# Kernel tuning notes

Hardware: AMD Instinct MI355X
Metric: run time of the kernel (lower is better)

The kernel has to match this reference:

```python
import jax, jax.numpy as jnp
import numpy as np

EXTENT = 1.0  # kernel-point influence radius (init kwarg 'extent')
B, N, M, H, K, F, C = 4, 16384, 16384, 32, 15, 64, 64


def setup_inputs() -> dict:
    key = jax.random.key(0)
    ks = jax.random.split(key, 6)
    points = jax.random.uniform(ks[0], (B, N, 3), dtype=jnp.float32)
    features = jax.random.normal(ks[1], (B, N, F), dtype=jnp.float32)
    output_points = jax.random.uniform(ks[2], (B, M, 3), dtype=jnp.float32)
    neighbor_indices = jax.random.randint(ks[3], (B, M, H), 0, N)
    # kernel point dispositions inside a ball of radius 1.5*extent (load_kernels stand-in)
    k_points = jax.random.uniform(ks[4], (K, 3), minval=-1.0, maxval=1.0, dtype=jnp.float32) * (1.5 * EXTENT) / jnp.sqrt(3.0)
    k_values = jax.random.normal(ks[5], (K, F, C), dtype=jnp.float32) * 0.05
    return {
        'points': points, 'features': features, 'output_points': output_points,
        'k_points': k_points, 'k_values': k_values, 'neighbor_indices': neighbor_indices,
    }


def reference(points, features, output_points, k_points, k_values, neighbor_indices):
    b, m, h = neighbor_indices.shape
    idx = neighbor_indices.reshape(b, m * h, 1)
    # batched gather (tf.gather batch_dims=1)
    neigh_pts = jnp.take_along_axis(points, idx, axis=1).reshape(b, m, h, 3)
    neigh_feat = jnp.take_along_axis(features, idx, axis=1).reshape(b, m, h, -1)
    # relative coords to each output point, then to each kernel point
    rel = neigh_pts - output_points[:, :, None, :]                # [B,M,H,3]
    diff = rel[:, :, :, None, :] - k_points                       # [B,M,H,K,3]
    sq_d = jnp.sum(diff * diff, axis=-1)                          # [B,M,H,K]
    # linear influence
    w = jnp.maximum(1.0 - jnp.sqrt(sq_d) / EXTENT, 0.0)           # [B,M,H,K]
    # weight neighbor features per kernel point, then apply per-kernel linear map, sum over K
    wf = jnp.einsum('bmhk,bmhf->bmkf', w, neigh_feat)             # [B,M,K,F]
    out = jnp.einsum('bmkf,kfc->bmc', wf, k_values)               # [B,M,C]
    return out
```

## Files before the change

### kernel.cpp

```cpp
#include <hip/hip_runtime.h>

#define BATCH 4
#define NPTS 16384
#define MPTS 16384
#define NH 32
#define NK 15
#define NF 64
#define NC 64
#define MT 16

typedef short short8 __attribute__((ext_vector_type(8)));
typedef float floatx4 __attribute__((ext_vector_type(4)));

__device__ __forceinline__ unsigned short f2bf(float x) {
    unsigned int u = __builtin_bit_cast(unsigned int, x);
    u = u + 0x7FFFu + ((u >> 16) & 1u);
    return (unsigned short)(u >> 16);
}

__device__ __forceinline__ unsigned pack_trunc(float lo, float hi) {
    return __builtin_amdgcn_perm(__builtin_bit_cast(unsigned, hi),
                                 __builtin_bit_cast(unsigned, lo), 0x07060302u);
}

__global__ void prep_kernel(const float* __restrict__ kv, const float* __restrict__ feat,
                            unsigned short* __restrict__ vp, unsigned short* __restrict__ featbf) {
    if (blockIdx.x < 32) {
        const int gid = blockIdx.x * 256 + threadIdx.x;
        const int lane = gid & 63;
        const int ct   = (gid >> 6) & 3;
        const int kk   = gid >> 8;
        const int c    = ct * 16 + (lane & 15);
        const int kap0 = kk * 32 + (lane >> 4) * 8;
        unsigned int o[4];
        #pragma unroll
        for (int jj = 0; jj < 4; jj++) {
            unsigned short lo, hi;
            {
                const int kap = kap0 + jj * 2;
                const int f = kap >> 4, k = kap & 15;
                lo = (k < NK) ? f2bf(kv[((size_t)(k * NF + f)) * NC + c]) : (unsigned short)0;
            }
            {
                const int kap = kap0 + jj * 2 + 1;
                const int f = kap >> 4, k = kap & 15;
                hi = (k < NK) ? f2bf(kv[((size_t)(k * NF + f)) * NC + c]) : (unsigned short)0;
            }
            o[jj] = (unsigned)lo | ((unsigned)hi << 16);
        }
        *(uint4*)(vp + (size_t)gid * 8) = make_uint4(o[0], o[1], o[2], o[3]);
    } else {
        const int gid = (blockIdx.x - 32) * 256 + threadIdx.x;
        const size_t base = (size_t)gid * 8;
        float4 a = *(const float4*)(feat + base);
        float4 b = *(const float4*)(feat + base + 4);
        uint4 o;
        o.x = (unsigned)f2bf(a.x) | ((unsigned)f2bf(a.y) << 16);
        o.y = (unsigned)f2bf(a.z) | ((unsigned)f2bf(a.w) << 16);
        o.z = (unsigned)f2bf(b.x) | ((unsigned)f2bf(b.y) << 16);
        o.w = (unsigned)f2bf(b.z) | ((unsigned)f2bf(b.w) << 16);
        *(uint4*)(featbf + base) = o;
    }
}

__global__ __launch_bounds__(256, 5) void kpconv_kernel(
    const float* __restrict__ points,
    const unsigned short* __restrict__ featbf,
    const float* __restrict__ outpts,
    const float* __restrict__ kpts,
    const unsigned short* __restrict__ vp,
    const int*   __restrict__ nbr,
    float* __restrict__ out)
{
    __shared__ __align__(16) unsigned short awf[16 * 512];
    __shared__ unsigned short feat_s[4 * 1288];
    __shared__ int   idx_s[512];
    __shared__ float opt_s[48];
    __shared__ float kp_s[48];

    const int tid   = threadIdx.x;
    const int batch = blockIdx.x >> 10;
    const int m0    = (blockIdx.x & 1023) << 4;

    if (tid < 48) kp_s[tid] = (tid < 45) ? kpts[tid] : 1e9f;
    if (tid >= 64 && tid < 112)
        opt_s[tid - 64] = outpts[(size_t)(batch * MPTS + m0) * 3 + (tid - 64)];
    {
        const size_t nb = (size_t)(batch * MPTS + m0) * NH;
        idx_s[tid]       = nbr[nb + tid];
        idx_s[256 + tid] = nbr[nb + 256 + tid];
    }
    __syncthreads();

    const int g    = tid >> 6;
    const int lane = tid & 63;
    const int cl   = lane & 15;
    const int q    = lane >> 4;
    const int sa   = cl;
    const int sfc  = q;

    const unsigned short* fbase = featbf + (size_t)(batch * NPTS) * NF;

    uint4 pra, prb;
    {
        const int srow = g * 32 + sa * 2;
        const int id0 = idx_s[srow], id1 = idx_s[srow + 1];
        pra = *(const uint4*)(fbase + (size_t)id0 * NF + sfc * 8);
        prb = *(const uint4*)(fbase + (size_t)id1 * NF + sfc * 8);
    }

    float4* rel4 = (float4*)awf;
    #pragma unroll
    for (int rr = 0; rr < 2; rr++) {
        const int row = tid * 2 + rr;
        const int id  = idx_s[row];
        const int pm  = row >> 5;
        const float* pp = points + ((size_t)(batch * NPTS) + id) * 3;
        rel4[row] = make_float4(pp[0] - opt_s[pm * 3 + 0],
                                pp[1] - opt_s[pm * 3 + 1],
                                pp[2] - opt_s[pm * 3 + 2], 0.f);
    }
    __syncthreads();

    short8 af[4];
    {
        const float kx = kp_s[cl * 3 + 0];
        const float ky = kp_s[cl * 3 + 1];
        const float kz = kp_s[cl * 3 + 2];
        #pragma unroll
        for (int rp = 0; rp < 4; rp++) {
            const int p = rp * 4 + g;
            float wv[8];
            #pragma unroll
            for (int j = 0; j < 8; j++) {
                const float4 rr = rel4[p * 32 + q * 8 + j];
                const float dx = rr.x - kx, dy = rr.y - ky, dz = rr.z - kz;
                const float d = sqrtf(dx * dx + dy * dy + dz * dz);
                wv[j] = fmaxf(1.f - d, 0.f);
            }
            uint4 ua;
            ua.x = pack_trunc(wv[0], wv[1]);
            ua.y = pack_trunc(wv[2], wv[3]);
            ua.z = pack_trunc(wv[4], wv[5]);
            ua.w = pack_trunc(wv[6], wv[7]);
            af[rp] = __builtin_bit_cast(short8, ua);
        }
    }
    __syncthreads();

    floatx4 acc0 = {0.f, 0.f, 0.f, 0.f};
    floatx4 acc1 = {0.f, 0.f, 0.f, 0.f};
    const unsigned short* vpg = vp + g * 512 + lane * 8;
    unsigned short* dp = &feat_s[g * 1288 + (sfc * 8) * 40 + sa * 2];

    #pragma unroll
    for (int it = 0; it < 8; it++) {
        const int r  = it & 3;
        const int p  = r * 4 + g;

        *(unsigned*)(dp + 0 * 40) = __builtin_amdgcn_perm(prb.x, pra.x, 0x05040100u);
        *(unsigned*)(dp + 1 * 40) = __builtin_amdgcn_perm(prb.x, pra.x, 0x07060302u);
        *(unsigned*)(dp + 2 * 40) = __builtin_amdgcn_perm(prb.y, pra.y, 0x05040100u);
        *(unsigned*)(dp + 3 * 40) = __builtin_amdgcn_perm(prb.y, pra.y, 0x07060302u);
        *(unsigned*)(dp + 4 * 40) = __builtin_amdgcn_perm(prb.z, pra.z, 0x05040100u);
        *(unsigned*)(dp + 5 * 40) = __builtin_amdgcn_perm(prb.z, pra.z, 0x07060302u);
        *(unsigned*)(dp + 6 * 40) = __builtin_amdgcn_perm(prb.w, pra.w, 0x05040100u);
        *(unsigned*)(dp + 7 * 40) = __builtin_amdgcn_perm(prb.w, pra.w, 0x07060302u);

        if (it < 7) {
            const int nit = it + 1;
            const int nfh = nit >> 2, nr = nit & 3;
            const int srow = (nr * 4 + g) * 32 + sa * 2;
            const int id0 = idx_s[srow], id1 = idx_s[srow + 1];
            pra = *(const uint4*)(fbase + (size_t)id0 * NF + nfh * 32 + sfc * 8);
            prb = *(const uint4*)(fbase + (size_t)id1 * NF + nfh * 32 + sfc * 8);
        }

        #pragma unroll
        for (int t = 0; t < 2; t++) {
            const uint4 ub = *(const uint4*)&feat_s[g * 1288 + (t * 16 + cl) * 40 + q * 8];
            floatx4 dd = {0.f, 0.f, 0.f, 0.f};
            dd = __builtin_amdgcn_mfma_f32_16x16x32_bf16(af[r], __builtin_bit_cast(short8, ub), dd, 0, 0, 0);
            const int kk    = 8 * t + (cl >> 1);
            const int q2    = (2 * cl + (q >> 1)) & 3;
            const int chunk = (p ^ kk) | (q2 << 4);
            unsigned* wp = (unsigned*)awf + kk * 256 + chunk * 4 + (q & 1) * 2;
            wp[0] = pack_trunc(dd[0], dd[1]);
            wp[1] = pack_trunc(dd[2], dd[3]);
        }

        if (it == 3) {
            __syncthreads();
            #pragma unroll 4
            for (int kk = 0; kk < 16; kk++) {
                const int chunk = (cl ^ kk) | (lane & 48);
                const uint4 uA = *(const uint4*)&awf[kk * 512 + chunk * 8];
                const uint4 uB = *(const uint4*)(vpg + (size_t)kk * 2048);
                if (kk & 1)
                    acc1 = __builtin_amdgcn_mfma_f32_16x16x32_bf16(
                        __builtin_bit_cast(short8, uA), __builtin_bit_cast(short8, uB), acc1, 0, 0, 0);
                else
                    acc0 = __builtin_amdgcn_mfma_f32_16x16x32_bf16(
                        __builtin_bit_cast(short8, uA), __builtin_bit_cast(short8, uB), acc0, 0, 0, 0);
            }
            __syncthreads();
        }
    }

    __syncthreads();
    #pragma unroll 4
    for (int kk = 0; kk < 16; kk++) {
        const int chunk = (cl ^ kk) | (lane & 48);
        const uint4 uA = *(const uint4*)&awf[kk * 512 + chunk * 8];
        const uint4 uB = *(const uint4*)(vpg + (size_t)(16 + kk) * 2048);
        if (kk & 1)
            acc1 = __builtin_amdgcn_mfma_f32_16x16x32_bf16(
                __builtin_bit_cast(short8, uA), __builtin_bit_cast(short8, uB), acc1, 0, 0, 0);
        else
            acc0 = __builtin_amdgcn_mfma_f32_16x16x32_bf16(
                __builtin_bit_cast(short8, uA), __builtin_bit_cast(short8, uB), acc0, 0, 0, 0);
    }
    const floatx4 acc = acc0 + acc1;

    #pragma unroll
    for (int ri = 0; ri < 4; ri++) {
        out[((size_t)(batch * MPTS + m0 + q * 4 + ri)) * NC + g * 16 + cl] = acc[ri];
    }
}

extern "C" void kernel_launch(void* const* d_in, const int* in_sizes, int n_in,
                              void* d_out, int out_size, void* d_ws, size_t ws_size,
                              hipStream_t stream) {
    const float* points   = (const float*)d_in[0];
    const float* features = (const float*)d_in[1];
    const float* outpts   = (const float*)d_in[2];
    const float* kpts     = (const float*)d_in[3];
    const float* kvals    = (const float*)d_in[4];
    const int*   nbr      = (const int*)d_in[5];
    float* out = (float*)d_out;

    unsigned short* vp     = (unsigned short*)d_ws;
    unsigned short* featbf = (unsigned short*)((char*)d_ws + 131072);

    prep_kernel<<<2080, 256, 0, stream>>>(kvals, features, vp, featbf);

    const int blocks = BATCH * (MPTS / MT);
    kpconv_kernel<<<blocks, 256, 0, stream>>>(points, featbf, outpts, kpts, vp, nbr, out);
}
```

Baseline: 143.5 us.

## Gather fp32 features directly in main kernel, drop bf16 feature prep pass

Removes the separate pass that converted all features to bf16 in workspace; the main kernel now gathers fp32 features directly and truncates them to bf16 while writing to shared memory. Neighbor indices, output points and kernel points are loaded straight into registers per wave instead of staged through shared memory, removing two block barriers. It also remaps point rows so each wave handles four consecutive output points, software-prefetches kernel-value tiles before the MFMA loops, and raises the occupancy hint to 6. The trade-off is that gathers now move twice the bytes per neighbor (fp32 vs bf16) in exchange for skipping the full feature conversion pass, and feature rounding changes from round-to-nearest to truncation.

```diff
diff --git a/kernel.cpp b/kernel.cpp
--- a/kernel.cpp
+++ b/kernel.cpp
@@ -7,7 +7,6 @@
 #define NK 15
 #define NF 64
 #define NC 64
-#define MT 16
 
 typedef short short8 __attribute__((ext_vector_type(8)));
 typedef float floatx4 __attribute__((ext_vector_type(4)));
@@ -23,49 +22,35 @@
                                  __builtin_bit_cast(unsigned, lo), 0x07060302u);
 }
 
-__global__ void prep_kernel(const float* __restrict__ kv, const float* __restrict__ feat,
-                            unsigned short* __restrict__ vp, unsigned short* __restrict__ featbf) {
-    if (blockIdx.x < 32) {
-        const int gid = blockIdx.x * 256 + threadIdx.x;
-        const int lane = gid & 63;
-        const int ct   = (gid >> 6) & 3;
-        const int kk   = gid >> 8;
-        const int c    = ct * 16 + (lane & 15);
-        const int kap0 = kk * 32 + (lane >> 4) * 8;
-        unsigned int o[4];
-        #pragma unroll
-        for (int jj = 0; jj < 4; jj++) {
-            unsigned short lo, hi;
-            {
-                const int kap = kap0 + jj * 2;
-                const int f = kap >> 4, k = kap & 15;
-                lo = (k < NK) ? f2bf(kv[((size_t)(k * NF + f)) * NC + c]) : (unsigned short)0;
-            }
-            {
-                const int kap = kap0 + jj * 2 + 1;
-                const int f = kap >> 4, k = kap & 15;
-                hi = (k < NK) ? f2bf(kv[((size_t)(k * NF + f)) * NC + c]) : (unsigned short)0;
-            }
-            o[jj] = (unsigned)lo | ((unsigned)hi << 16);
-        }
-        *(uint4*)(vp + (size_t)gid * 8) = make_uint4(o[0], o[1], o[2], o[3]);
-    } else {
-        const int gid = (blockIdx.x - 32) * 256 + threadIdx.x;
-        const size_t base = (size_t)gid * 8;
-        float4 a = *(const float4*)(feat + base);
-        float4 b = *(const float4*)(feat + base + 4);
-        uint4 o;
-        o.x = (unsigned)f2bf(a.x) | ((unsigned)f2bf(a.y) << 16);
-        o.y = (unsigned)f2bf(a.z) | ((unsigned)f2bf(a.w) << 16);
-        o.z = (unsigned)f2bf(b.x) | ((unsigned)f2bf(b.y) << 16);
-        o.w = (unsigned)f2bf(b.z) | ((unsigned)f2bf(b.w) << 16);
-        *(uint4*)(featbf + base) = o;
-    }
-}
-
-__global__ __launch_bounds__(256, 5) void kpconv_kernel(
+__global__ void vprep_kernel(const float* __restrict__ kv, unsigned short* __restrict__ vp) {
+    const int gid = blockIdx.x * 256 + threadIdx.x;
+    const int lane = gid & 63;
+    const int ct   = (gid >> 6) & 3;
+    const int kk   = gid >> 8;
+    const int c    = ct * 16 + (lane & 15);
+    const int kap0 = kk * 32 + (lane >> 4) * 8;
+    unsigned int o[4];
+    #pragma unroll
+    for (int jj = 0; jj < 4; jj++) {
+        unsigned short lo, hi;
+        {
+            const int kap = kap0 + jj * 2;
+            const int f = kap >> 4, k = kap & 15;
+            lo = (k < NK) ? f2bf(kv[((size_t)(k * NF + f)) * NC + c]) : (unsigned short)0;
+        }
+        {
+            const int kap = kap0 + jj * 2 + 1;
+            const int f = kap >> 4, k = kap & 15;
+            hi = (k < NK) ? f2bf(kv[((size_t)(k * NF + f)) * NC + c]) : (unsigned short)0;
+        }
+        o[jj] = (unsigned)lo | ((unsigned)hi << 16);
+    }
+    *(uint4*)(vp + (size_t)gid * 8) = make_uint4(o[0], o[1], o[2], o[3]);
+}
+
+__global__ __launch_bounds__(256, 6) void kpconv_kernel(
     const float* __restrict__ points,
-    const unsigned short* __restrict__ featbf,
+    const float* __restrict__ features,
     const float* __restrict__ outpts,
     const float* __restrict__ kpts,
     const unsigned short* __restrict__ vp,
@@ -73,155 +58,135 @@
     float* __restrict__ out)
 {
     __shared__ __align__(16) unsigned short awf[16 * 512];
-    __shared__ unsigned short feat_s[4 * 1288];
-    __shared__ int   idx_s[512];
-    __shared__ float opt_s[48];
-    __shared__ float kp_s[48];
+    __shared__ __align__(16) unsigned short feat_s[4 * 1312];
 
     const int tid   = threadIdx.x;
+    const int g     = tid >> 6;
+    const int lane  = tid & 63;
+    const int cl    = lane & 15;
+    const int q     = lane >> 4;
     const int batch = blockIdx.x >> 10;
     const int m0    = (blockIdx.x & 1023) << 4;
-
-    if (tid < 48) kp_s[tid] = (tid < 45) ? kpts[tid] : 1e9f;
-    if (tid >= 64 && tid < 112)
-        opt_s[tid - 64] = outpts[(size_t)(batch * MPTS + m0) * 3 + (tid - 64)];
+    const int pbase = batch * MPTS + m0 + 4 * g;
+
+    int2 sid[4];
     {
-        const size_t nb = (size_t)(batch * MPTS + m0) * NH;
-        idx_s[tid]       = nbr[nb + tid];
-        idx_s[256 + tid] = nbr[nb + 256 + tid];
-    }
-    __syncthreads();
-
-    const int g    = tid >> 6;
-    const int lane = tid & 63;
-    const int cl   = lane & 15;
-    const int q    = lane >> 4;
-    const int sa   = cl;
-    const int sfc  = q;
-
-    const unsigned short* fbase = featbf + (size_t)(batch * NPTS) * NF;
-
-    uint4 pra, prb;
+        const int* nb = nbr + (size_t)pbase * NH + 2 * cl;
+        #pragma unroll
+        for (int r = 0; r < 4; r++) sid[r] = *(const int2*)(nb + r * NH);
+    }
+
+    const float* fb = features + (size_t)(batch * NPTS) * NF;
+
+    float4 gaL, gaH, gbL, gbH;
     {
-        const int srow = g * 32 + sa * 2;
-        const int id0 = idx_s[srow], id1 = idx_s[srow + 1];
-        pra = *(const uint4*)(fbase + (size_t)id0 * NF + sfc * 8);
-        prb = *(const uint4*)(fbase + (size_t)id1 * NF + sfc * 8);
+        const float* fa = fb + (size_t)sid[0].x * NF + q * 8;
+        const float* fc = fb + (size_t)sid[0].y * NF + q * 8;
+        gaL = *(const float4*)fa;       gaH = *(const float4*)(fa + 4);
+        gbL = *(const float4*)fc;       gbH = *(const float4*)(fc + 4);
     }
 
     float4* rel4 = (float4*)awf;
-    #pragma unroll
-    for (int rr = 0; rr < 2; rr++) {
-        const int row = tid * 2 + rr;
-        const int id  = idx_s[row];
-        const int pm  = row >> 5;
-        const float* pp = points + ((size_t)(batch * NPTS) + id) * 3;
-        rel4[row] = make_float4(pp[0] - opt_s[pm * 3 + 0],
-                                pp[1] - opt_s[pm * 3 + 1],
-                                pp[2] - opt_s[pm * 3 + 2], 0.f);
-    }
-    __syncthreads();
+    {
+        const float* ob = outpts + (size_t)(pbase + q) * 3;
+        const float ox = ob[0], oy = ob[1], oz = ob[2];
+        const float* pp = points + (size_t)(batch * NPTS) * 3;
+        const float* p0 = pp + (size_t)sid[q].x * 3;
+        const float* p1 = pp + (size_t)sid[q].y * 3;
+        rel4[128 * g + 32 * q + 2 * cl    ] = make_float4(p0[0] - ox, p0[1] - oy, p0[2] - oz, 0.f);
+        rel4[128 * g + 32 * q + 2 * cl + 1] = make_float4(p1[0] - ox, p1[1] - oy, p1[2] - oz, 0.f);
+    }
+
+    float kx, ky, kz;
+    if (cl < NK) { kx = kpts[cl * 3]; ky = kpts[cl * 3 + 1]; kz = kpts[cl * 3 + 2]; }
+    else         { kx = 1e9f; ky = 1e9f; kz = 1e9f; }
 
     short8 af[4];
-    {
-        const float kx = kp_s[cl * 3 + 0];
-        const float ky = kp_s[cl * 3 + 1];
-        const float kz = kp_s[cl * 3 + 2];
-        #pragma unroll
-        for (int rp = 0; rp < 4; rp++) {
-            const int p = rp * 4 + g;
-            float wv[8];
-            #pragma unroll
-            for (int j = 0; j < 8; j++) {
-                const float4 rr = rel4[p * 32 + q * 8 + j];
-                const float dx = rr.x - kx, dy = rr.y - ky, dz = rr.z - kz;
-                const float d = sqrtf(dx * dx + dy * dy + dz * dz);
-                wv[j] = fmaxf(1.f - d, 0.f);
-            }
-            uint4 ua;
-            ua.x = pack_trunc(wv[0], wv[1]);
-            ua.y = pack_trunc(wv[2], wv[3]);
-            ua.z = pack_trunc(wv[4], wv[5]);
-            ua.w = pack_trunc(wv[6], wv[7]);
-            af[rp] = __builtin_bit_cast(short8, ua);
-        }
+    #pragma unroll
+    for (int rp = 0; rp < 4; rp++) {
+        float wv[8];
+        #pragma unroll
+        for (int j = 0; j < 8; j++) {
+            const float4 rr = rel4[128 * g + 32 * rp + q * 8 + j];
+            const float dx = rr.x - kx, dy = rr.y - ky, dz = rr.z - kz;
+            wv[j] = fmaxf(1.f - sqrtf(dx * dx + dy * dy + dz * dz), 0.f);
+        }
+        uint4 ua;
+        ua.x = pack_trunc(wv[0], wv[1]);
+        ua.y = pack_trunc(wv[2], wv[3]);
+        ua.z = pack_trunc(wv[4], wv[5]);
+        ua.w = pack_trunc(wv[6], wv[7]);
+        af[rp] = __builtin_bit_cast(short8, ua);
     }
     __syncthreads();
 
     floatx4 acc0 = {0.f, 0.f, 0.f, 0.f};
     floatx4 acc1 = {0.f, 0.f, 0.f, 0.f};
     const unsigned short* vpg = vp + g * 512 + lane * 8;
-    unsigned short* dp = &feat_s[g * 1288 + (sfc * 8) * 40 + sa * 2];
-
-    #pragma unroll
-    for (int it = 0; it < 8; it++) {
-        const int r  = it & 3;
-        const int p  = r * 4 + g;
-
-        *(unsigned*)(dp + 0 * 40) = __builtin_amdgcn_perm(prb.x, pra.x, 0x05040100u);
-        *(unsigned*)(dp + 1 * 40) = __builtin_amdgcn_perm(prb.x, pra.x, 0x07060302u);
-        *(unsigned*)(dp + 2 * 40) = __builtin_amdgcn_perm(prb.y, pra.y, 0x05040100u);
-        *(unsigned*)(dp + 3 * 40) = __builtin_amdgcn_perm(prb.y, pra.y, 0x07060302u);
-        *(unsigned*)(dp + 4 * 40) = __builtin_amdgcn_perm(prb.z, pra.z, 0x05040100u);
-        *(unsigned*)(dp + 5 * 40) = __builtin_amdgcn_perm(prb.z, pra.z, 0x07060302u);
-        *(unsigned*)(dp + 6 * 40) = __builtin_amdgcn_perm(prb.w, pra.w, 0x05040100u);
-        *(unsigned*)(dp + 7 * 40) = __builtin_amdgcn_perm(prb.w, pra.w, 0x07060302u);
-
-        if (it < 7) {
-            const int nit = it + 1;
-            const int nfh = nit >> 2, nr = nit & 3;
-            const int srow = (nr * 4 + g) * 32 + sa * 2;
-            const int id0 = idx_s[srow], id1 = idx_s[srow + 1];
-            pra = *(const uint4*)(fbase + (size_t)id0 * NF + nfh * 32 + sfc * 8);
-            prb = *(const uint4*)(fbase + (size_t)id1 * NF + nfh * 32 + sfc * 8);
-        }
-
-        #pragma unroll
-        for (int t = 0; t < 2; t++) {
-            const uint4 ub = *(const uint4*)&feat_s[g * 1288 + (t * 16 + cl) * 40 + q * 8];
-            floatx4 dd = {0.f, 0.f, 0.f, 0.f};
-            dd = __builtin_amdgcn_mfma_f32_16x16x32_bf16(af[r], __builtin_bit_cast(short8, ub), dd, 0, 0, 0);
-            const int kk    = 8 * t + (cl >> 1);
-            const int q2    = (2 * cl + (q >> 1)) & 3;
-            const int chunk = (p ^ kk) | (q2 << 4);
-            unsigned* wp = (unsigned*)awf + kk * 256 + chunk * 4 + (q & 1) * 2;
-            wp[0] = pack_trunc(dd[0], dd[1]);
-            wp[1] = pack_trunc(dd[2], dd[3]);
-        }
-
-        if (it == 3) {
-            __syncthreads();
-            #pragma unroll 4
-            for (int kk = 0; kk < 16; kk++) {
-                const int chunk = (cl ^ kk) | (lane & 48);
-                const uint4 uA = *(const uint4*)&awf[kk * 512 + chunk * 8];
-                const uint4 uB = *(const uint4*)(vpg + (size_t)kk * 2048);
-                if (kk & 1)
-                    acc1 = __builtin_amdgcn_mfma_f32_16x16x32_bf16(
-                        __builtin_bit_cast(short8, uA), __builtin_bit_cast(short8, uB), acc1, 0, 0, 0);
-                else
-                    acc0 = __builtin_amdgcn_mfma_f32_16x16x32_bf16(
-                        __builtin_bit_cast(short8, uA), __builtin_bit_cast(short8, uB), acc0, 0, 0, 0);
+    unsigned short* dpw = feat_s + g * 1312 + q * 328 + 2 * cl;
+
+    #pragma unroll
+    for (int fh = 0; fh < 2; fh++) {
+        #pragma unroll
+        for (int r = 0; r < 4; r++) {
+            const int p = 4 * g + r;
+
+            *(unsigned*)(dpw + 0 * 40) = pack_trunc(gaL.x, gbL.x);
+            *(unsigned*)(dpw + 1 * 40) = pack_trunc(gaL.y, gbL.y);
+            *(unsigned*)(dpw + 2 * 40) = pack_trunc(gaL.z, gbL.z);
+            *(unsigned*)(dpw + 3 * 40) = pack_trunc(gaL.w, gbL.w);
+            *(unsigned*)(dpw + 4 * 40) = pack_trunc(gaH.x, gbH.x);
+            *(unsigned*)(dpw + 5 * 40) = pack_trunc(gaH.y, gbH.y);
+            *(unsigned*)(dpw + 6 * 40) = pack_trunc(gaH.z, gbH.z);
+            *(unsigned*)(dpw + 7 * 40) = pack_trunc(gaH.w, gbH.w);
+
+            if (!(fh == 1 && r == 3)) {
+                const int nit = fh * 4 + r + 1;
+                const int nfh = nit >> 2, nr = nit & 3;
+                const float* fa = fb + (size_t)sid[nr].x * NF + nfh * 32 + q * 8;
+                const float* fc = fb + (size_t)sid[nr].y * NF + nfh * 32 + q * 8;
+                gaL = *(const float4*)fa;       gaH = *(const float4*)(fa + 4);
+                gbL = *(const float4*)fc;       gbH = *(const float4*)(fc + 4);
             }
-            __syncthreads();
-        }
-    }
-
-    __syncthreads();
-    #pragma unroll 4
-    for (int kk = 0; kk < 16; kk++) {
-        const int chunk = (cl ^ kk) | (lane & 48);
-        const uint4 uA = *(const uint4*)&awf[kk * 512 + chunk * 8];
-        const uint4 uB = *(const uint4*)(vpg + (size_t)(16 + kk) * 2048);
-        if (kk & 1)
-            acc1 = __builtin_amdgcn_mfma_f32_16x16x32_bf16(
-                __builtin_bit_cast(short8, uA), __builtin_bit_cast(short8, uB), acc1, 0, 0, 0);
-        else
-            acc0 = __builtin_amdgcn_mfma_f32_16x16x32_bf16(
-                __builtin_bit_cast(short8, uA), __builtin_bit_cast(short8, uB), acc0, 0, 0, 0);
-    }
+
+            #pragma unroll
+            for (int t = 0; t < 2; t++) {
+                const unsigned short* brd =
+                    feat_s + g * 1312 + (2 * t + (cl >> 3)) * 328 + (cl & 7) * 40 + q * 8;
+                const uint4 ub = *(const uint4*)brd;
+                floatx4 dd = {0.f, 0.f, 0.f, 0.f};
+                dd = __builtin_amdgcn_mfma_f32_16x16x32_bf16(
+                    af[r], __builtin_bit_cast(short8, ub), dd, 0, 0, 0);
+                const int kk    = 8 * t + (cl >> 1);
+                const int q2    = (2 * cl + (q >> 1)) & 3;
+                const int chunk = (p ^ kk) | (q2 << 4);
+                unsigned* wp = (unsigned*)awf + kk * 256 + chunk * 4 + (q & 1) * 2;
+                wp[0] = pack_trunc(dd[0], dd[1]);
+                wp[1] = pack_trunc(dd[2], dd[3]);
+            }
+        }
+
+        uint4 v0 = *(const uint4*)(vpg + (size_t)(fh * 16 + 0) * 2048);
+        uint4 v1 = *(const uint4*)(vpg + (size_t)(fh * 16 + 1) * 2048);
+        __syncthreads();
+        #pragma unroll
+        for (int kk = 0; kk < 16; kk++) {
+            const int chunk = (cl ^ kk) | (lane & 48);
+            const uint4 uA = *(const uint4*)&awf[kk * 512 + chunk * 8];
+            const uint4 uB = v0;
+            v0 = v1;
+            if (kk < 14) v1 = *(const uint4*)(vpg + (size_t)(fh * 16 + kk + 2) * 2048);
+            if (kk & 1)
+                acc1 = __builtin_amdgcn_mfma_f32_16x16x32_bf16(
+                    __builtin_bit_cast(short8, uA), __builtin_bit_cast(short8, uB), acc1, 0, 0, 0);
+            else
+                acc0 = __builtin_amdgcn_mfma_f32_16x16x32_bf16(
+                    __builtin_bit_cast(short8, uA), __builtin_bit_cast(short8, uB), acc0, 0, 0, 0);
+        }
+        if (fh == 0) __syncthreads();
+    }
+
     const floatx4 acc = acc0 + acc1;
-
     #pragma unroll
     for (int ri = 0; ri < 4; ri++) {
         out[((size_t)(batch * MPTS + m0 + q * 4 + ri)) * NC + g * 16 + cl] = acc[ri];
@@ -239,11 +204,10 @@
     const int*   nbr      = (const int*)d_in[5];
     float* out = (float*)d_out;
 
-    unsigned short* vp     = (unsigned short*)d_ws;
-    unsigned short* featbf = (unsigned short*)((char*)d_ws + 131072);
-
-    prep_kernel<<<2080, 256, 0, stream>>>(kvals, features, vp, featbf);
-
-    const int blocks = BATCH * (MPTS / MT);
-    kpconv_kernel<<<blocks, 256, 0, stream>>>(points, featbf, outpts, kpts, vp, nbr, out);
-}
+    unsigned short* vp = (unsigned short*)d_ws;
+
+    vprep_kernel<<<32, 256, 0, stream>>>(kvals, vp);
+
+    const int blocks = BATCH * (MPTS / 16);
+    kpconv_kernel<<<blocks, 256, 0, stream>>>(points, features, outpts, kpts, vp, nbr, out);
+}
```

Measured after the change: 187.9 us. +30.9%, slower.
